# Kernel optimization log

Measured on AMD Instinct MI355X. Metric: run time of the kernel, lower is better.

Reference implementation:

```python
import jax, jax.numpy as jnp
import numpy as np

B, T, C = 2, 2048, 2048
NH, NKV = 16, 4
HD = C // NH  # 128


def setup_inputs() -> dict:
    key = jax.random.key(0)
    ks = jax.random.split(key, 5)
    w = lambda k, shape: jax.random.normal(k, shape, jnp.float32) * 0.02
    return {
        "x": jax.random.normal(ks[0], (B, T, C), jnp.float32),
        "Wq": w(ks[1], (C, C)),
        "Wk": w(ks[2], (C, NKV * HD)),
        "Wv": w(ks[3], (C, NKV * HD)),
        "Wproj": w(ks[4], (C, C)),
    }


def _rope(x):
    # x: [B, H, T, D]; rotate-half RoPE with base 10000
    D = x.shape[-1]
    t = x.shape[-2]
    inv_freq = 1.0 / (10000.0 ** (jnp.arange(0, D, 2, dtype=jnp.float32) / D))
    freqs = jnp.arange(t, dtype=jnp.float32)[:, None] * inv_freq[None, :]  # [T, D/2]
    emb = jnp.concatenate([freqs, freqs], axis=-1)  # [T, D]
    cos, sin = jnp.cos(emb), jnp.sin(emb)
    x1, x2 = x[..., : D // 2], x[..., D // 2 :]
    rotated = jnp.concatenate([-x2, x1], axis=-1)
    return x * cos + rotated * sin


def reference(x, Wq, Wk, Wv, Wproj):
    b, t, c = x.shape
    q = (x @ Wq).reshape(b, t, NH, HD).transpose(0, 2, 1, 3)    # [B,NH,T,HD]
    k = (x @ Wk).reshape(b, t, NKV, HD).transpose(0, 2, 1, 3)   # [B,NKV,T,HD]
    v = (x @ Wv).reshape(b, t, NKV, HD).transpose(0, 2, 1, 3)
    q = _rope(q)
    k = _rope(k)
    rep = NH // NKV
    k = jnp.repeat(k, rep, axis=1)  # [B,NH,T,HD]
    v = jnp.repeat(v, rep, axis=1)
    scale = 1.0 / jnp.sqrt(jnp.float32(HD))
    scores = jnp.einsum("bhqd,bhkd->bhqk", q, k) * scale        # [B,NH,T,T]
    causal = jnp.tril(jnp.ones((t, t), dtype=bool))
    scores = jnp.where(causal, scores, jnp.finfo(scores.dtype).min)
    attn = jax.nn.softmax(scores, axis=-1)
    y = jnp.einsum("bhqk,bhkd->bhqd", attn, v)                  # [B,NH,T,HD]
    y = y.transpose(0, 2, 1, 3).reshape(b, t, c)
    return y @ Wproj
```

## Files before the change

### kernel.cpp

```cpp
#include <hip/hip_runtime.h>

#define B_ 2
#define T_ 2048
#define C_ 2048
#define NH_ 16
#define NKV_ 4
#define HD_ 128
#define M_ 4096
#define NQKV_ 3072

typedef __bf16 bf16x8 __attribute__((ext_vector_type(8)));
typedef float f32x4 __attribute__((ext_vector_type(4)));
typedef float f32x16 __attribute__((ext_vector_type(16)));

__device__ __forceinline__ unsigned short f2bf(float f) {
  union { float f; unsigned u; } c{f};
  unsigned u = c.u + 0x7FFFu + ((c.u >> 16) & 1u);
  return (unsigned short)(u >> 16);
}
__device__ __forceinline__ float bf2f(unsigned short h) {
  union { unsigned u; float f; } c{(unsigned)h << 16};
  return c.f;
}

#define GLOAD_LDS16(g, l)                                        \
  __builtin_amdgcn_global_load_lds(                              \
      (const __attribute__((address_space(1))) void*)(g),        \
      (__attribute__((address_space(3))) void*)(l), 16, 0, 0)

__device__ __forceinline__ bf16x8 ldsread128(const unsigned short* p) {
  uint4 d;
  asm volatile("ds_read_b128 %0, %1"
               : "=v"(d)
               : "v"((const __attribute__((address_space(3))) void*)p));
  union { uint4 u; bf16x8 v; } c;
  c.u = d;
  return c.v;
}

__global__ void prep_kernel(const float* __restrict__ x, const float* __restrict__ Wq,
                            const float* __restrict__ Wk, const float* __restrict__ Wv,
                            const float* __restrict__ Wp, unsigned short* __restrict__ xb,
                            unsigned short* __restrict__ wt, float2* __restrict__ rt) {
  int id = blockIdx.x;
  if (id < 10240) {
    __shared__ float tile[32][33];
    const float* W;
    unsigned short* Wt;
    int N, bx, by;
    if (id < 4096)      { W = Wq; Wt = wt;                       N = 2048; int u = id;        bx = u & 63; by = u >> 6; }
    else if (id < 5120) { W = Wk; Wt = wt + (size_t)2048 * 2048; N = 512;  int u = id - 4096; bx = u & 15; by = u >> 4; }
    else if (id < 6144) { W = Wv; Wt = wt + (size_t)2560 * 2048; N = 512;  int u = id - 5120; bx = u & 15; by = u >> 4; }
    else                { W = Wp; Wt = wt + (size_t)3072 * 2048; N = 2048; int u = id - 6144; bx = u & 63; by = u >> 6; }
    const int K = 2048;
    bx *= 32; by *= 32;
    int tx = threadIdx.x & 31, ty = threadIdx.x >> 5;
#pragma unroll
    for (int r = 0; r < 32; r += 8)
      tile[ty + r][tx] = W[(size_t)(by + ty + r) * N + bx + tx];
    __syncthreads();
#pragma unroll
    for (int r = 0; r < 32; r += 8)
      Wt[(size_t)(bx + ty + r) * K + by + tx] = f2bf(tile[tx][ty + r]);
  } else if (id < 18432) {
    int i = (id - 10240) * 256 + threadIdx.x;
    float4 v = reinterpret_cast<const float4*>(x)[i];
    union { ushort4 u; unsigned short s[4]; } o;
    o.s[0] = f2bf(v.x); o.s[1] = f2bf(v.y); o.s[2] = f2bf(v.z); o.s[3] = f2bf(v.w);
    reinterpret_cast<ushort4*>(xb)[i] = o.u;
  } else {
    int g = (id - 18432) * 256 + threadIdx.x;
    int t = g >> 6, i = g & 63;
    float inv = powf(10000.f, -(float)(2 * i) / 128.f);
    float s, c;
    sincosf((float)t * inv, &s, &c);
    rt[t * 64 + i] = make_float2(c, s);
  }
}

__global__ void transpose_v_kernel(const unsigned short* __restrict__ qkv,
                                   unsigned short* __restrict__ vt) {
  __shared__ unsigned short tile[32][33];
  int bh = blockIdx.z;
  int b = bh >> 2, kvh = bh & 3;
  int t0 = blockIdx.x * 32, d0 = blockIdx.y * 32;
  int tx = threadIdx.x & 31, ty = threadIdx.x >> 5;
#pragma unroll
  for (int r = 0; r < 32; r += 8)
    tile[ty + r][tx] = qkv[(size_t)(b * T_ + t0 + ty + r) * NQKV_ + 2560 + kvh * HD_ + d0 + tx];
  __syncthreads();
#pragma unroll
  for (int r = 0; r < 32; r += 8)
    vt[(size_t)(bh * HD_ + d0 + ty + r) * T_ + t0 + tx] = tile[tx][ty + r];
}

template <int BM, typename OUT, bool ROPE>
__global__ __launch_bounds__(512, 1) void gemm8p(const unsigned short* __restrict__ A,
                                                 const unsigned short* __restrict__ Bt,
                                                 OUT* __restrict__ Cm,
                                                 const float2* __restrict__ rt,
                                                 int M, int N, int K) {
  constexpr int MR = BM / 64;
  __shared__ __align__(16) unsigned short As[2][2][BM * 32];
  __shared__ __align__(16) unsigned short Bs[2][2][256 * 32];
  int tid = threadIdx.x, wid = tid >> 6, lane = tid & 63;
  int l15 = lane & 15, l4 = lane >> 4;
  int wr = wid >> 1, wc = wid & 1;
  size_t arow0 = (size_t)blockIdx.y * BM;
  size_t brow0 = (size_t)blockIdx.x * 256;
  int tmax = K / 64 - 1;

  f32x4 acc[MR][8];
#pragma unroll
  for (int m = 0; m < MR; ++m)
#pragma unroll
    for (int n = 0; n < 8; ++n) acc[m][n] = (f32x4){0.f, 0.f, 0.f, 0.f};

  auto stageA = [&](int slot, int kh, int tile) {
    int k0 = tile * 64 + kh * 32;
    constexpr int NLD = (BM * 32 * 2) / (512 * 16);
#pragma unroll
    for (int i = 0; i < NLD; ++i) {
      int c = i * 512 + wid * 64 + lane;
      int rg = c >> 2, cg = (c & 3) ^ (rg & 3);
      const unsigned short* g = A + (arow0 + rg) * K + k0 + cg * 8;
      GLOAD_LDS16(g, &As[slot][kh][c * 8]);
    }
  };
  auto stageB = [&](int slot, int kh, int tile) {
    int k0 = tile * 64 + kh * 32;
#pragma unroll
    for (int i = 0; i < 2; ++i) {
      int c = i * 512 + wid * 64 + lane;
      int rg = c >> 2, cg = (c & 3) ^ (rg & 3);
      const unsigned short* g = Bt + (brow0 + rg) * K + k0 + cg * 8;
      GLOAD_LDS16(g, &Bs[slot][kh][c * 8]);
    }
  };

  stageA(0, 0, 0); stageB(0, 0, 0); stageA(0, 1, 0); stageB(0, 1, 0);
  stageA(1, 0, 1); stageB(1, 0, 1); stageA(1, 1, 1);
  if constexpr (BM == 256) asm volatile("s_waitcnt vmcnt(6)" ::: "memory");
  else                     asm volatile("s_waitcnt vmcnt(4)" ::: "memory");
  __builtin_amdgcn_s_barrier();

  int NT2 = K / 128;
  for (int it = 0; it < NT2; ++it) {
    int t2 = it * 2;
#pragma unroll
    for (int tt = 0; tt < 2; ++tt) {
      bf16x8 af[MR];
#pragma unroll
      for (int kh = 0; kh < 2; ++kh) {
#pragma unroll
        for (int nh = 0; nh < 2; ++nh) {
          int p = tt * 4 + kh * 2 + nh + 1;
          if (nh == 0) {
#pragma unroll
            for (int m = 0; m < MR; ++m) {
              int r = wr * (MR * 16) + m * 16 + l15;
              af[m] = ldsread128(&As[tt][kh][r * 32 + ((l4 ^ (r & 3)) * 8)]);
            }
          }
          bf16x8 bf[4];
#pragma unroll
          for (int j = 0; j < 4; ++j) {
            int r = wc * 128 + (nh * 4 + j) * 16 + l15;
            bf[j] = ldsread128(&Bs[tt][kh][r * 32 + ((l4 ^ (r & 3)) * 8)]);
          }
          if (p == 1) stageB(1, 1, t2 + 1);
          if (p == 2) stageA(0, 0, t2 + 2 <= tmax ? t2 + 2 : tmax);
          if (p == 3) stageB(0, 0, t2 + 2 <= tmax ? t2 + 2 : tmax);
          if (p == 4) stageA(0, 1, t2 + 2 <= tmax ? t2 + 2 : tmax);
          if (p == 5) stageB(0, 1, t2 + 2 <= tmax ? t2 + 2 : tmax);
          if (p == 6) stageA(1, 0, t2 + 3 <= tmax ? t2 + 3 : tmax);
          if (p == 7) stageB(1, 0, t2 + 3 <= tmax ? t2 + 3 : tmax);
          if (p == 8) stageA(1, 1, t2 + 3 <= tmax ? t2 + 3 : tmax);

          __builtin_amdgcn_s_barrier();
          asm volatile("s_waitcnt lgkmcnt(0)" ::: "memory");
          __builtin_amdgcn_sched_barrier(0);
          __builtin_amdgcn_s_setprio(1);
#pragma unroll
          for (int m = 0; m < MR; ++m)
#pragma unroll
            for (int j = 0; j < 4; ++j)
              acc[m][nh * 4 + j] = __builtin_amdgcn_mfma_f32_16x16x32_bf16(
                  af[m], bf[j], acc[m][nh * 4 + j], 0, 0, 0);
          __builtin_amdgcn_s_setprio(0);
          if (p == 4 || p == 8) {
            if constexpr (BM == 256) asm volatile("s_waitcnt vmcnt(6)" ::: "memory");
            else                     asm volatile("s_waitcnt vmcnt(4)" ::: "memory");
          }
          __builtin_amdgcn_s_barrier();
        }
      }
    }
  }

  bool dorope = ROPE && (brow0 + wc * 128 < 2560);
#pragma unroll
  for (int m = 0; m < MR; ++m)
#pragma unroll
    for (int r = 0; r < 4; ++r) {
      size_t row = arow0 + wr * (MR * 16) + m * 16 + l4 * 4 + r;
      if (dorope) {
        int t = (int)(row & (T_ - 1));
#pragma unroll
        for (int n = 0; n < 4; ++n) {
          float2 cs = rt[t * 64 + n * 16 + l15];
          float a1 = acc[m][n][r], a2 = acc[m][n + 4][r];
          size_t col = brow0 + wc * 128 + n * 16 + l15;
          Cm[row * N + col]      = f2bf(a1 * cs.x - a2 * cs.y);
          Cm[row * N + col + 64] = f2bf(a2 * cs.x + a1 * cs.y);
        }
      } else {
#pragma unroll
        for (int n = 0; n < 8; ++n) {
          size_t col = brow0 + wc * 128 + n * 16 + l15;
          float v = acc[m][n][r];
          if constexpr (sizeof(OUT) == 4) Cm[row * N + col] = v;
          else                            Cm[row * N + col] = f2bf(v);
        }
      }
    }
}

__global__ __launch_bounds__(256, 2) void attn_kernel(const unsigned short* __restrict__ qkv,
                                                      const unsigned short* __restrict__ vt,
                                                      unsigned short* __restrict__ att,
                                                      unsigned short* __restrict__ pO,
                                                      float2* __restrict__ ml) {
  constexpr int KB = 64;
  __shared__ __align__(16) unsigned short Kl[2][KB * 128];
  __shared__ __align__(16) unsigned short Vl[2][128 * KB];
  int tid = threadIdx.x, w = tid >> 6, lane = tid & 63;
  int l31 = lane & 31, hi = lane >> 5;
  int h4 = hi * 4;

  int id = blockIdx.x;
  int qi, bh, kt0, kt1, slot = -1;
  if (id < 64) {
    qi = 9 - (id >> 5); bh = id & 31; kt0 = 0; kt1 = 2 * qi + 2;
  } else if (id < 448) {
    int s = id - 64;
    int pairidx = s >> 1, hihalf = s & 1;
    qi = 15 - (pairidx >> 5); bh = pairidx & 31;
    int nt = 2 * qi + 2, h = nt >> 1;
    kt0 = hihalf ? h : 0; kt1 = hihalf ? nt : h;
    slot = s;
  } else {
    int u = id - 448;
    qi = 7 - (u >> 5); bh = u & 31; kt0 = 0; kt1 = 2 * qi + 2;
  }
  int q0 = qi * 128;
  int b = bh >> 4, hd = bh & 15, kvh = hd >> 2;
  int qr0 = q0 + w * 32;
  int ql = qr0 + l31;

  bf16x8 qf[8];
  {
    const unsigned short* qb = qkv + (size_t)(b * T_ + ql) * NQKV_ + hd * HD_ + hi * 8;
    const float scale = 0.08838834764831845f * 1.4426950408889634f;
#pragma unroll
    for (int df = 0; df < 8; ++df) {
      bf16x8 t = *reinterpret_cast<const bf16x8*>(qb + df * 16);
#pragma unroll
      for (int j = 0; j < 8; ++j) t[j] = (__bf16)((float)t[j] * scale);
      qf[df] = t;
    }
  }

  f32x16 o[4];
#pragma unroll
  for (int dt = 0; dt < 4; ++dt)
#pragma unroll
    for (int r = 0; r < 16; ++r) o[dt][r] = 0.f;
  float mr = -1e30f, lr = 0.f;

  auto stage = [&](int buf, int kv0) {
#pragma unroll
    for (int i = 0; i < 4; ++i) {
      int c = (i * 4 + w) * 64 + lane;
      int g = c ^ ((c >> 4) & 7);
      const unsigned short* src =
          qkv + (size_t)(b * T_ + kv0 + (g >> 4)) * NQKV_ + C_ + kvh * HD_ + (g & 15) * 8;
      GLOAD_LDS16(src, &Kl[buf][(i * 4 + w) * 512]);
    }
#pragma unroll
    for (int i = 0; i < 4; ++i) {
      int c = (i * 4 + w) * 64 + lane;
      int g = c ^ ((c >> 3) & 7);
      const unsigned short* src =
          vt + (size_t)((b * NKV_ + kvh) * HD_ + (g >> 3)) * T_ + kv0 + (g & 7) * 8;
      GLOAD_LDS16(src, &Vl[buf][(i * 4 + w) * 512]);
    }
  };

  stage(0, kt0 * KB);
  __syncthreads();
  int cur = 0;
  for (int kt = kt0; kt < kt1; ++kt) {
    int kv0 = kt * KB;
    if (kt + 1 < kt1) stage(cur ^ 1, kv0 + KB);

    if (kv0 <= qr0 + 31) {
      f32x16 s[2];
#pragma unroll
      for (int r = 0; r < 16; ++r) { s[0][r] = 0.f; s[1][r] = 0.f; }
      const unsigned short* Kb = &Kl[cur][0];
      __builtin_amdgcn_s_setprio(1);
#pragma unroll
      for (int t2 = 0; t2 < 2; ++t2)
#pragma unroll
        for (int df = 0; df < 8; ++df) {
          bf16x8 kf = *reinterpret_cast<const bf16x8*>(
              Kb + (((t2 * 32 + l31) * 128 + df * 16 + hi * 8) ^ ((l31 & 7) << 3)));
          s[t2] = __builtin_amdgcn_mfma_f32_32x32x16_bf16(kf, qf[df], s[t2], 0, 0, 0);
        }
      __builtin_amdgcn_s_setprio(0);

      float rm = -1e30f;
      if ((kv0 + KB - 1) > qr0) {
#pragma unroll
        for (int t2 = 0; t2 < 2; ++t2)
#pragma unroll
          for (int r = 0; r < 16; ++r) {
            float sv = s[t2][r];
            int kcol = kv0 + t2 * 32 + (r & 3) + 8 * (r >> 2) + h4;
            if (kcol > ql) sv = -1e30f;
            s[t2][r] = sv;
            rm = fmaxf(rm, sv);
          }
      } else {
#pragma unroll
        for (int t2 = 0; t2 < 2; ++t2)
#pragma unroll
          for (int r = 0; r < 16; ++r) rm = fmaxf(rm, s[t2][r]);
      }
      rm = fmaxf(rm, __shfl_xor(rm, 32));

      if (!__all(rm <= mr + 11.0f)) {
        float mnew = fmaxf(mr, rm);
        float alpha = exp2f(mr - mnew);
        mr = mnew;
        lr *= alpha;
#pragma unroll
        for (int dt = 0; dt < 4; ++dt)
#pragma unroll
          for (int r = 0; r < 16; ++r) o[dt][r] *= alpha;
      }

      float ps = 0.f;
#pragma unroll
      for (int t2 = 0; t2 < 2; ++t2)
#pragma unroll
        for (int r = 0; r < 16; ++r) {
          float p = exp2f(s[t2][r] - mr);
          s[t2][r] = p;
          ps += p;
        }
      lr += ps;

      unsigned pk[2][8];
#pragma unroll
      for (int t2 = 0; t2 < 2; ++t2)
#pragma unroll
        for (int i = 0; i < 8; ++i) {
          union { unsigned u32; __bf16 hh[2]; } pr;
          pr.hh[0] = (__bf16)s[t2][2 * i];
          pr.hh[1] = (__bf16)s[t2][2 * i + 1];
          pk[t2][i] = pr.u32;
        }

      bf16x8 pb[4];
#pragma unroll
      for (int f = 0; f < 4; ++f) {
        int t2 = f >> 1, bq = (f & 1) * 4;
        union { bf16x8 v; unsigned d[4]; } fr;
#pragma unroll
        for (int p = 0; p < 2; ++p) {
          unsigned uu = pk[t2][bq + p];
          unsigned ww = pk[t2][bq + 2 + p];
          unsigned us = (unsigned)__shfl_xor((int)uu, 32);
          unsigned ws = (unsigned)__shfl_xor((int)ww, 32);
          fr.d[p]     = hi ? ws : uu;
          fr.d[2 + p] = hi ? ww : us;
        }
        pb[f] = fr.v;
      }

      const unsigned short* Vb = &Vl[cur][0];
      __builtin_amdgcn_s_setprio(1);
#pragma unroll
      for (int dt = 0; dt < 4; ++dt)
#pragma unroll
        for (int kf = 0; kf < 4; ++kf) {
          bf16x8 vf = *reinterpret_cast<const bf16x8*>(
              Vb + (((dt * 32 + l31) * KB + kf * 16 + hi * 8) ^ ((l31 & 7) << 3)));
          o[dt] = __builtin_amdgcn_mfma_f32_32x32x16_bf16(vf, pb[kf], o[dt], 0, 0, 0);
        }
      __builtin_amdgcn_s_setprio(0);
    }

    __syncthreads();
    cur ^= 1;
  }

  float ls = lr + __shfl_xor(lr, 32);
  if (slot < 0) {
    float inv = 1.f / ls;
    unsigned short* ob = att + (size_t)(b * T_ + ql) * C_ + hd * HD_;
#pragma unroll
    for (int dt = 0; dt < 4; ++dt)
#pragma unroll
      for (int r = 0; r < 16; ++r) {
        int d = dt * 32 + (r & 3) + 8 * (r >> 2) + h4;
        ob[d] = f2bf(o[dt][r] * inv);
      }
  } else {
    int lrow = w * 32 + l31;
    unsigned short* po = pO + (size_t)slot * 16384 + lrow * 128;
#pragma unroll
    for (int dt = 0; dt < 4; ++dt)
#pragma unroll
      for (int r = 0; r < 16; ++r) {
        int d = dt * 32 + (r & 3) + 8 * (r >> 2) + h4;
        po[d] = f2bf(o[dt][r]);
      }
    if (hi == 0) ml[slot * 128 + lrow] = make_float2(mr, ls);
  }
}

__global__ void combine_kernel(const unsigned short* __restrict__ pO,
                               const float2* __restrict__ ml,
                               unsigned short* __restrict__ att) {
  int pairidx = blockIdx.x;
  int qi = 15 - (pairidx >> 5), bh = pairidx & 31;
  int b = bh >> 4, hd = bh & 15;
  int q0 = qi * 128;
  int s0 = pairidx * 2, s1 = s0 + 1;
  int tid = threadIdx.x;
  int row = tid >> 1, dh = (tid & 1) * 64;
  float2 ml0 = ml[s0 * 128 + row], ml1 = ml[s1 * 128 + row];
  float m = fmaxf(ml0.x, ml1.x);
  float w0 = exp2f(ml0.x - m), w1 = exp2f(ml1.x - m);
  float inv = 1.f / (w0 * ml0.y + w1 * ml1.y);
  const unsigned short* p0 = pO + (size_t)s0 * 16384 + row * 128 + dh;
  const unsigned short* p1 = pO + (size_t)s1 * 16384 + row * 128 + dh;
  unsigned short* ob = att + (size_t)(b * T_ + q0 + row) * C_ + hd * HD_ + dh;
#pragma unroll
  for (int j = 0; j < 64; j += 4) {
    ushort4 a = *reinterpret_cast<const ushort4*>(p0 + j);
    ushort4 c = *reinterpret_cast<const ushort4*>(p1 + j);
    ushort4 r;
    r.x = f2bf((w0 * bf2f(a.x) + w1 * bf2f(c.x)) * inv);
    r.y = f2bf((w0 * bf2f(a.y) + w1 * bf2f(c.y)) * inv);
    r.z = f2bf((w0 * bf2f(a.z) + w1 * bf2f(c.z)) * inv);
    r.w = f2bf((w0 * bf2f(a.w) + w1 * bf2f(c.w)) * inv);
    *reinterpret_cast<ushort4*>(ob + j) = r;
  }
}

extern "C" void kernel_launch(void* const* d_in, const int* in_sizes, int n_in,
                              void* d_out, int out_size, void* d_ws, size_t ws_size,
                              hipStream_t stream) {
  const float* x  = (const float*)d_in[0];
  const float* Wq = (const float*)d_in[1];
  const float* Wk = (const float*)d_in[2];
  const float* Wv = (const float*)d_in[3];
  const float* Wp = (const float*)d_in[4];
  float* out = (float*)d_out;
  char* ws = (char*)d_ws;

  unsigned short* xb  = (unsigned short*)(ws);
  unsigned short* wt  = (unsigned short*)(ws + 16777216);
  unsigned short* qkv = (unsigned short*)(ws + 37748736);
  float2*         rt  = (float2*)(ws + 62914560);
  unsigned short* vt  = (unsigned short*)(ws + 63963136);
  unsigned short* att = xb;
  unsigned short* pO  = wt;
  float2*         ml  = rt;

  prep_kernel<<<dim3(18944), 256, 0, stream>>>(x, Wq, Wk, Wv, Wp, xb, wt, rt);

  gemm8p<256, unsigned short, true><<<dim3(NQKV_ / 256, M_ / 256), 512, 0, stream>>>(
      xb, wt, qkv, rt, M_, NQKV_, C_);
  transpose_v_kernel<<<dim3(T_ / 32, HD_ / 32, B_ * NKV_), 256, 0, stream>>>(qkv, vt);
  attn_kernel<<<dim3(704), 256, 0, stream>>>(qkv, vt, att, pO, ml);
  combine_kernel<<<dim3(192), 256, 0, stream>>>(pO, ml, att);
  gemm8p<128, float, false><<<dim3(C_ / 256, M_ / 128), 512, 0, stream>>>(
      att, wt + (size_t)3072 * 2048, out, nullptr, M_, C_, C_);
}
```

Baseline: 214.0 us.

## Read V fragments directly from global in MFMA-ready layout, drop V LDS staging

The V transpose kernel now writes V in a packed layout where each lane's 8-element bf16 MFMA operand is contiguous. The attention kernel drops its V shared-memory buffer and loads V fragments straight from global/L2 into registers, double-buffered across the four output tiles. The P-fragment shuffle is replaced by v_permlane32_swap, and the launch bound no longer pins two blocks per CU. This removes LDS traffic and halves LDS footprint, but exposes global-load latency inside the PV loop and may raise register pressure.

```diff
diff --git a/kernel.cpp b/kernel.cpp
--- a/kernel.cpp
+++ b/kernel.cpp
@@ -79,19 +79,30 @@
 }
 
 __global__ void transpose_v_kernel(const unsigned short* __restrict__ qkv,
-                                   unsigned short* __restrict__ vt) {
-  __shared__ unsigned short tile[32][33];
-  int bh = blockIdx.z;
+                                   unsigned short* __restrict__ vt2) {
+  __shared__ unsigned short tile[64][136];
+  int bt = blockIdx.x;
+  int bh = bt >> 5, t = bt & 31;
   int b = bh >> 2, kvh = bh & 3;
-  int t0 = blockIdx.x * 32, d0 = blockIdx.y * 32;
-  int tx = threadIdx.x & 31, ty = threadIdx.x >> 5;
-#pragma unroll
-  for (int r = 0; r < 32; r += 8)
-    tile[ty + r][tx] = qkv[(size_t)(b * T_ + t0 + ty + r) * NQKV_ + 2560 + kvh * HD_ + d0 + tx];
+  int tid = threadIdx.x;
+#pragma unroll
+  for (int p = 0; p < 4; ++p) {
+    int kv = p * 16 + (tid >> 4);
+    int c8 = (tid & 15) * 8;
+    *reinterpret_cast<uint4*>(&tile[kv][c8]) = *reinterpret_cast<const uint4*>(
+        &qkv[(size_t)(b * T_ + t * 64 + kv) * NQKV_ + 2560 + kvh * HD_ + c8]);
+  }
   __syncthreads();
 #pragma unroll
-  for (int r = 0; r < 32; r += 8)
-    vt[(size_t)(bh * HD_ + d0 + ty + r) * T_ + t0 + tx] = tile[tx][ty + r];
+  for (int it = 0; it < 4; ++it) {
+    int item = it * 256 + tid;
+    int pk = item >> 7, d = item & 127;
+    unsigned short tmp[8];
+#pragma unroll
+    for (int j = 0; j < 8; ++j) tmp[j] = tile[pk * 8 + j][d];
+    *reinterpret_cast<uint4*>(&vt2[((size_t)(bt * 8 + pk) * 128 + d) * 8]) =
+        *reinterpret_cast<uint4*>(tmp);
+  }
 }
 
 template <int BM, typename OUT, bool ROPE>
@@ -226,14 +237,13 @@
     }
 }
 
-__global__ __launch_bounds__(256, 2) void attn_kernel(const unsigned short* __restrict__ qkv,
-                                                      const unsigned short* __restrict__ vt,
-                                                      unsigned short* __restrict__ att,
-                                                      unsigned short* __restrict__ pO,
-                                                      float2* __restrict__ ml) {
+__global__ __launch_bounds__(256) void attn_kernel(const unsigned short* __restrict__ qkv,
+                                                   const unsigned short* __restrict__ vt2,
+                                                   unsigned short* __restrict__ att,
+                                                   unsigned short* __restrict__ pO,
+                                                   float2* __restrict__ ml) {
   constexpr int KB = 64;
   __shared__ __align__(16) unsigned short Kl[2][KB * 128];
-  __shared__ __align__(16) unsigned short Vl[2][128 * KB];
   int tid = threadIdx.x, w = tid >> 6, lane = tid & 63;
   int l31 = lane & 31, hi = lane >> 5;
   int h4 = hi * 4;
@@ -287,15 +297,10 @@
           qkv + (size_t)(b * T_ + kv0 + (g >> 4)) * NQKV_ + C_ + kvh * HD_ + (g & 15) * 8;
       GLOAD_LDS16(src, &Kl[buf][(i * 4 + w) * 512]);
     }
-#pragma unroll
-    for (int i = 0; i < 4; ++i) {
-      int c = (i * 4 + w) * 64 + lane;
-      int g = c ^ ((c >> 3) & 7);
-      const unsigned short* src =
-          vt + (size_t)((b * NKV_ + kvh) * HD_ + (g >> 3)) * T_ + kv0 + (g & 7) * 8;
-      GLOAD_LDS16(src, &Vl[buf][(i * 4 + w) * 512]);
-    }
   };
+
+  const unsigned short* vb = vt2 + (size_t)((b * NKV_ + kvh) * 32) * 8192;
+  union Vc { uint4 u; bf16x8 v; };
 
   stage(0, kt0 * KB);
   __syncthreads();
@@ -373,6 +378,15 @@
           pk[t2][i] = pr.u32;
         }
 
+      const unsigned short* vbt = vb + (size_t)kt * 8192;
+      uint4 va[4], vc[4];
+#pragma unroll
+      for (int kf = 0; kf < 4; ++kf)
+        va[kf] = *reinterpret_cast<const uint4*>(vbt + ((kf * 2 + hi) * 128 + l31) * 8);
+#pragma unroll
+      for (int kf = 0; kf < 4; ++kf)
+        vc[kf] = *reinterpret_cast<const uint4*>(vbt + ((kf * 2 + hi) * 128 + 32 + l31) * 8);
+
       bf16x8 pb[4];
 #pragma unroll
       for (int f = 0; f < 4; ++f) {
@@ -380,26 +394,42 @@
         union { bf16x8 v; unsigned d[4]; } fr;
 #pragma unroll
         for (int p = 0; p < 2; ++p) {
-          unsigned uu = pk[t2][bq + p];
-          unsigned ww = pk[t2][bq + 2 + p];
-          unsigned us = (unsigned)__shfl_xor((int)uu, 32);
-          unsigned ws = (unsigned)__shfl_xor((int)ww, 32);
-          fr.d[p]     = hi ? ws : uu;
-          fr.d[2 + p] = hi ? ww : us;
+          unsigned a = pk[t2][bq + p];
+          unsigned bb2 = pk[t2][bq + 2 + p];
+          asm("v_permlane32_swap_b32 %0, %1" : "+v"(a), "+v"(bb2));
+          fr.d[p] = a;
+          fr.d[2 + p] = bb2;
         }
         pb[f] = fr.v;
       }
 
-      const unsigned short* Vb = &Vl[cur][0];
       __builtin_amdgcn_s_setprio(1);
 #pragma unroll
-      for (int dt = 0; dt < 4; ++dt)
-#pragma unroll
-        for (int kf = 0; kf < 4; ++kf) {
-          bf16x8 vf = *reinterpret_cast<const bf16x8*>(
-              Vb + (((dt * 32 + l31) * KB + kf * 16 + hi * 8) ^ ((l31 & 7) << 3)));
-          o[dt] = __builtin_amdgcn_mfma_f32_32x32x16_bf16(vf, pb[kf], o[dt], 0, 0, 0);
-        }
+      for (int kf = 0; kf < 4; ++kf) {
+        Vc c; c.u = va[kf];
+        o[0] = __builtin_amdgcn_mfma_f32_32x32x16_bf16(c.v, pb[kf], o[0], 0, 0, 0);
+      }
+#pragma unroll
+      for (int kf = 0; kf < 4; ++kf)
+        va[kf] = *reinterpret_cast<const uint4*>(vbt + ((kf * 2 + hi) * 128 + 64 + l31) * 8);
+#pragma unroll
+      for (int kf = 0; kf < 4; ++kf) {
+        Vc c; c.u = vc[kf];
+        o[1] = __builtin_amdgcn_mfma_f32_32x32x16_bf16(c.v, pb[kf], o[1], 0, 0, 0);
+      }
+#pragma unroll
+      for (int kf = 0; kf < 4; ++kf)
+        vc[kf] = *reinterpret_cast<const uint4*>(vbt + ((kf * 2 + hi) * 128 + 96 + l31) * 8);
+#pragma unroll
+      for (int kf = 0; kf < 4; ++kf) {
+        Vc c; c.u = va[kf];
+        o[2] = __builtin_amdgcn_mfma_f32_32x32x16_bf16(c.v, pb[kf], o[2], 0, 0, 0);
+      }
+#pragma unroll
+      for (int kf = 0; kf < 4; ++kf) {
+        Vc c; c.u = vc[kf];
+        o[3] = __builtin_amdgcn_mfma_f32_32x32x16_bf16(c.v, pb[kf], o[3], 0, 0, 0);
+      }
       __builtin_amdgcn_s_setprio(0);
     }
 
@@ -477,7 +507,7 @@
   unsigned short* wt  = (unsigned short*)(ws + 16777216);
   unsigned short* qkv = (unsigned short*)(ws + 37748736);
   float2*         rt  = (float2*)(ws + 62914560);
-  unsigned short* vt  = (unsigned short*)(ws + 63963136);
+  unsigned short* vt2 = (unsigned short*)(ws + 63963136);
   unsigned short* att = xb;
   unsigned short* pO  = wt;
   float2*         ml  = rt;
@@ -486,8 +516,8 @@
 
   gemm8p<256, unsigned short, true><<<dim3(NQKV_ / 256, M_ / 256), 512, 0, stream>>>(
       xb, wt, qkv, rt, M_, NQKV_, C_);
-  transpose_v_kernel<<<dim3(T_ / 32, HD_ / 32, B_ * NKV_), 256, 0, stream>>>(qkv, vt);
-  attn_kernel<<<dim3(704), 256, 0, stream>>>(qkv, vt, att, pO, ml);
+  transpose_v_kernel<<<dim3(256), 256, 0, stream>>>(qkv, vt2);
+  attn_kernel<<<dim3(704), 256, 0, stream>>>(qkv, vt2, att, pO, ml);
   combine_kernel<<<dim3(192), 256, 0, stream>>>(pO, ml, att);
   gemm8p<128, float, false><<<dim3(C_ / 256, M_ / 128), 512, 0, stream>>>(
       att, wt + (size_t)3072 * 2048, out, nullptr, M_, C_, C_);
```

New measurement: 249.2 us. +16.5%, slower.

## Stage V through registers into a single LDS buffer and drop occupancy hint

Applied to the files above, without the earlier changes.

V tiles are now prefetched one tile ahead into registers with plain global loads and written into a single swizzled LDS buffer between the QK^T/softmax and PV phases. A mid-iteration barrier separates the two phases, K stays double-buffered via direct global-to-LDS loads, and the launch_bounds minimum of 2 blocks per CU is removed. The aim is to halve V's LDS footprint and overlap V's global latency with the score computation, at the cost of extra VGPRs, an extra barrier per tile, and a redundant reload of the last tile.

```diff
diff --git a/kernel.cpp b/kernel.cpp
--- a/kernel.cpp
+++ b/kernel.cpp
@@ -226,14 +226,14 @@
     }
 }
 
-__global__ __launch_bounds__(256, 2) void attn_kernel(const unsigned short* __restrict__ qkv,
-                                                      const unsigned short* __restrict__ vt,
-                                                      unsigned short* __restrict__ att,
-                                                      unsigned short* __restrict__ pO,
-                                                      float2* __restrict__ ml) {
+__global__ __launch_bounds__(256) void attn_kernel(const unsigned short* __restrict__ qkv,
+                                                   const unsigned short* __restrict__ vt,
+                                                   unsigned short* __restrict__ att,
+                                                   unsigned short* __restrict__ pO,
+                                                   float2* __restrict__ ml) {
   constexpr int KB = 64;
   __shared__ __align__(16) unsigned short Kl[2][KB * 128];
-  __shared__ __align__(16) unsigned short Vl[2][128 * KB];
+  __shared__ __align__(16) unsigned short Vl[128 * KB];
   int tid = threadIdx.x, w = tid >> 6, lane = tid & 63;
   int l31 = lane & 31, hi = lane >> 5;
   int h4 = hi * 4;
@@ -278,7 +278,8 @@
     for (int r = 0; r < 16; ++r) o[dt][r] = 0.f;
   float mr = -1e30f, lr = 0.f;
 
-  auto stage = [&](int buf, int kv0) {
+  auto stage_K = [&](int buf, int tile) {
+    int kv0 = tile * KB;
 #pragma unroll
     for (int i = 0; i < 4; ++i) {
       int c = (i * 4 + w) * 64 + lane;
@@ -287,24 +288,40 @@
           qkv + (size_t)(b * T_ + kv0 + (g >> 4)) * NQKV_ + C_ + kvh * HD_ + (g & 15) * 8;
       GLOAD_LDS16(src, &Kl[buf][(i * 4 + w) * 512]);
     }
+  };
+
+  uint4 vreg[4];
+  const unsigned short* vbase = vt + (size_t)((b * NKV_ + kvh) * HD_) * T_;
+  auto load_V = [&](int tile) {
+    int kv0 = tile * KB;
 #pragma unroll
     for (int i = 0; i < 4; ++i) {
-      int c = (i * 4 + w) * 64 + lane;
-      int g = c ^ ((c >> 3) & 7);
-      const unsigned short* src =
-          vt + (size_t)((b * NKV_ + kvh) * HD_ + (g >> 3)) * T_ + kv0 + (g & 7) * 8;
-      GLOAD_LDS16(src, &Vl[buf][(i * 4 + w) * 512]);
+      int d = w * 32 + i * 8 + (lane >> 3);
+      vreg[i] = *reinterpret_cast<const uint4*>(vbase + (size_t)d * T_ + kv0 + (lane & 7) * 8);
     }
   };
-
-  stage(0, kt0 * KB);
+  auto write_V = [&]() {
+#pragma unroll
+    for (int i = 0; i < 4; ++i) {
+      int d = w * 32 + i * 8 + (lane >> 3);
+      int kv8 = lane & 7;
+      *reinterpret_cast<uint4*>(&Vl[d * 64 + ((kv8 ^ (d & 7)) << 3)]) = vreg[i];
+    }
+  };
+
+  stage_K(0, kt0);
+  load_V(kt0);
   __syncthreads();
+
   int cur = 0;
   for (int kt = kt0; kt < kt1; ++kt) {
     int kv0 = kt * KB;
-    if (kt + 1 < kt1) stage(cur ^ 1, kv0 + KB);
-
-    if (kv0 <= qr0 + 31) {
+    int tn = kt + 1 < kt1 ? kt + 1 : kt1 - 1;
+    stage_K(cur ^ 1, tn);
+
+    bool active = (kv0 <= qr0 + 31);
+    unsigned pk[2][8];
+    if (active) {
       f32x16 s[2];
 #pragma unroll
       for (int r = 0; r < 16; ++r) { s[0][r] = 0.f; s[1][r] = 0.f; }
@@ -362,7 +379,6 @@
         }
       lr += ps;
 
-      unsigned pk[2][8];
 #pragma unroll
       for (int t2 = 0; t2 < 2; ++t2)
 #pragma unroll
@@ -372,7 +388,15 @@
           pr.hh[1] = (__bf16)s[t2][2 * i + 1];
           pk[t2][i] = pr.u32;
         }
-
+    }
+
+    write_V();
+    load_V(tn);
+    asm volatile("s_waitcnt lgkmcnt(0)" ::: "memory");
+    __builtin_amdgcn_s_barrier();
+    __builtin_amdgcn_sched_barrier(0);
+
+    if (active) {
       bf16x8 pb[4];
 #pragma unroll
       for (int f = 0; f < 4; ++f) {
@@ -390,14 +414,13 @@
         pb[f] = fr.v;
       }
 
-      const unsigned short* Vb = &Vl[cur][0];
       __builtin_amdgcn_s_setprio(1);
 #pragma unroll
       for (int dt = 0; dt < 4; ++dt)
 #pragma unroll
         for (int kf = 0; kf < 4; ++kf) {
           bf16x8 vf = *reinterpret_cast<const bf16x8*>(
-              Vb + (((dt * 32 + l31) * KB + kf * 16 + hi * 8) ^ ((l31 & 7) << 3)));
+              Vl + (((dt * 32 + l31) * KB + kf * 16 + hi * 8) ^ ((l31 & 7) << 3)));
           o[dt] = __builtin_amdgcn_mfma_f32_32x32x16_bf16(vf, pb[kf], o[dt], 0, 0, 0);
         }
       __builtin_amdgcn_s_setprio(0);
```

After: 282.5 us. 1.32x slower.

## Split more query tiles across blocks and interleave split/unsplit scheduling order

Applied to the files above, without the earlier changes.

The attention grid grows from 704 to 768 blocks. Query tiles 8-15 are now split into two KV halves, where before only tiles 10-15 were split, and the block order interleaves split long work with unsplit short work for better load balance. The first half writes its unnormalized partial output directly into the attention output buffer, so the combine kernel reads it back from there and needs only one scratch partial per pair. The cost is more blocks and a larger combine pass over 256 pairs.

```diff
diff --git a/kernel.cpp b/kernel.cpp
--- a/kernel.cpp
+++ b/kernel.cpp
@@ -239,19 +239,31 @@
   int h4 = hi * 4;
 
   int id = blockIdx.x;
-  int qi, bh, kt0, kt1, slot = -1;
-  if (id < 64) {
-    qi = 9 - (id >> 5); bh = id & 31; kt0 = 0; kt1 = 2 * qi + 2;
-  } else if (id < 448) {
-    int s = id - 64;
-    int pairidx = s >> 1, hihalf = s & 1;
-    qi = 15 - (pairidx >> 5); bh = pairidx & 31;
-    int nt = 2 * qi + 2, h = nt >> 1;
-    kt0 = hihalf ? h : 0; kt1 = hihalf ? nt : h;
-    slot = s;
+  bool split;
+  int qi, l;
+  if      (id < 64)  { split = true;  qi = 15; l = id; }
+  else if (id < 96)  { split = false; qi = 7;  l = id - 64; }
+  else if (id < 160) { split = true;  qi = 14; l = id - 96; }
+  else if (id < 224) { split = true;  qi = 13; l = id - 160; }
+  else if (id < 256) { split = false; qi = 6;  l = id - 224; }
+  else if (id < 320) { split = true;  qi = 12; l = id - 256; }
+  else if (id < 384) { split = true;  qi = 11; l = id - 320; }
+  else if (id < 416) { split = false; qi = 5;  l = id - 384; }
+  else if (id < 480) { split = true;  qi = 10; l = id - 416; }
+  else if (id < 544) { split = true;  qi = 9;  l = id - 480; }
+  else if (id < 576) { split = false; qi = 4;  l = id - 544; }
+  else if (id < 640) { split = true;  qi = 8;  l = id - 576; }
+  else if (id < 672) { split = false; qi = 3;  l = id - 640; }
+  else if (id < 704) { split = false; qi = 2;  l = id - 672; }
+  else if (id < 736) { split = false; qi = 1;  l = id - 704; }
+  else               { split = false; qi = 0;  l = id - 736; }
+  int bh, kt0, kt1, pair = -1, half = 0;
+  if (split) {
+    bh = l >> 1; half = l & 1; pair = (15 - qi) * 32 + bh;
+    int nt = 2 * qi + 2, h = qi + 1;
+    kt0 = half ? h : 0; kt1 = half ? nt : h;
   } else {
-    int u = id - 448;
-    qi = 7 - (u >> 5); bh = u & 31; kt0 = 0; kt1 = 2 * qi + 2;
+    bh = l; kt0 = 0; kt1 = 2 * qi + 2;
   }
   int q0 = qi * 128;
   int b = bh >> 4, hd = bh & 15, kvh = hd >> 2;
@@ -408,7 +420,7 @@
   }
 
   float ls = lr + __shfl_xor(lr, 32);
-  if (slot < 0) {
+  if (pair < 0) {
     float inv = 1.f / ls;
     unsigned short* ob = att + (size_t)(b * T_ + ql) * C_ + hd * HD_;
 #pragma unroll
@@ -418,9 +430,19 @@
         int d = dt * 32 + (r & 3) + 8 * (r >> 2) + h4;
         ob[d] = f2bf(o[dt][r] * inv);
       }
+  } else if (half == 0) {
+    unsigned short* ob = att + (size_t)(b * T_ + ql) * C_ + hd * HD_;
+#pragma unroll
+    for (int dt = 0; dt < 4; ++dt)
+#pragma unroll
+      for (int r = 0; r < 16; ++r) {
+        int d = dt * 32 + (r & 3) + 8 * (r >> 2) + h4;
+        ob[d] = f2bf(o[dt][r]);
+      }
+    if (hi == 0) ml[(pair * 2) * 128 + w * 32 + l31] = make_float2(mr, ls);
   } else {
     int lrow = w * 32 + l31;
-    unsigned short* po = pO + (size_t)slot * 16384 + lrow * 128;
+    unsigned short* po = pO + (size_t)pair * 16384 + lrow * 128;
 #pragma unroll
     for (int dt = 0; dt < 4; ++dt)
 #pragma unroll
@@ -428,30 +450,28 @@
         int d = dt * 32 + (r & 3) + 8 * (r >> 2) + h4;
         po[d] = f2bf(o[dt][r]);
       }
-    if (hi == 0) ml[slot * 128 + lrow] = make_float2(mr, ls);
+    if (hi == 0) ml[(pair * 2 + 1) * 128 + lrow] = make_float2(mr, ls);
   }
 }
 
 __global__ void combine_kernel(const unsigned short* __restrict__ pO,
                                const float2* __restrict__ ml,
                                unsigned short* __restrict__ att) {
-  int pairidx = blockIdx.x;
-  int qi = 15 - (pairidx >> 5), bh = pairidx & 31;
+  int pair = blockIdx.x;
+  int qi = 15 - (pair >> 5), bh = pair & 31;
   int b = bh >> 4, hd = bh & 15;
   int q0 = qi * 128;
-  int s0 = pairidx * 2, s1 = s0 + 1;
   int tid = threadIdx.x;
   int row = tid >> 1, dh = (tid & 1) * 64;
-  float2 ml0 = ml[s0 * 128 + row], ml1 = ml[s1 * 128 + row];
+  float2 ml0 = ml[(pair * 2) * 128 + row], ml1 = ml[(pair * 2 + 1) * 128 + row];
   float m = fmaxf(ml0.x, ml1.x);
   float w0 = exp2f(ml0.x - m), w1 = exp2f(ml1.x - m);
   float inv = 1.f / (w0 * ml0.y + w1 * ml1.y);
-  const unsigned short* p0 = pO + (size_t)s0 * 16384 + row * 128 + dh;
-  const unsigned short* p1 = pO + (size_t)s1 * 16384 + row * 128 + dh;
   unsigned short* ob = att + (size_t)(b * T_ + q0 + row) * C_ + hd * HD_ + dh;
+  const unsigned short* p1 = pO + (size_t)pair * 16384 + row * 128 + dh;
 #pragma unroll
   for (int j = 0; j < 64; j += 4) {
-    ushort4 a = *reinterpret_cast<const ushort4*>(p0 + j);
+    ushort4 a = *reinterpret_cast<const ushort4*>(ob + j);
     ushort4 c = *reinterpret_cast<const ushort4*>(p1 + j);
     ushort4 r;
     r.x = f2bf((w0 * bf2f(a.x) + w1 * bf2f(c.x)) * inv);
@@ -487,8 +507,8 @@
   gemm8p<256, unsigned short, true><<<dim3(NQKV_ / 256, M_ / 256), 512, 0, stream>>>(
       xb, wt, qkv, rt, M_, NQKV_, C_);
   transpose_v_kernel<<<dim3(T_ / 32, HD_ / 32, B_ * NKV_), 256, 0, stream>>>(qkv, vt);
-  attn_kernel<<<dim3(704), 256, 0, stream>>>(qkv, vt, att, pO, ml);
-  combine_kernel<<<dim3(192), 256, 0, stream>>>(pO, ml, att);
+  attn_kernel<<<dim3(768), 256, 0, stream>>>(qkv, vt, att, pO, ml);
+  combine_kernel<<<dim3(256), 256, 0, stream>>>(pO, ml, att);
   gemm8p<128, float, false><<<dim3(C_ / 256, M_ / 128), 512, 0, stream>>>(
       att, wt + (size_t)3072 * 2048, out, nullptr, M_, C_, C_);
 }
```

Measured after the change: 216.9 us. About the same (+1.4%).
